# Optimization experiments

Hardware: AMD Instinct MI355X
Metric: run time of the kernel (lower is better)

Reference implementation:

```python
import jax, jax.numpy as jnp
import numpy as np

N_NODES = 100000
N_EDGES = 3200000
IN_FEAT = 512
HIDDEN = 16
N_CLASSES = 7


def gcn_conv(x, src, dst, dinv, W, b, n):
    # x: [N, Fin], src/dst: [E+N] (self-loops appended), dinv: [E+N already-indexed? no]
    h = x @ W  # [N, Fout]
    norm = (dinv[src] * dinv[dst])[:, None]  # [E+N, 1]
    msg = h[src] * norm
    out = jax.ops.segment_sum(msg, dst, num_segments=n)
    return out + b


def setup_inputs() -> dict:
    key = jax.random.key(0)
    k1, k2, k3, k4 = jax.random.split(key, 4)
    x = jax.random.normal(k1, (N_NODES, IN_FEAT), dtype=jnp.float32)
    edge_index = jax.random.randint(k2, (2, N_EDGES), 0, N_NODES, dtype=jnp.int64)
    # Glorot-style init for GCNConv linear layers
    W1 = jax.random.normal(k3, (IN_FEAT, HIDDEN), dtype=jnp.float32) / np.sqrt(IN_FEAT)
    b1 = jnp.zeros((HIDDEN,), dtype=jnp.float32)
    W2 = jax.random.normal(k4, (HIDDEN, N_CLASSES), dtype=jnp.float32) / np.sqrt(HIDDEN)
    b2 = jnp.zeros((N_CLASSES,), dtype=jnp.float32)
    return {"x": x, "edge_index": edge_index, "W1": W1, "b1": b1, "W2": W2, "b2": b2}


def reference(x, edge_index, W1, b1, W2, b2):
    n = x.shape[0]
    loop = jnp.arange(n, dtype=edge_index.dtype)
    src = jnp.concatenate([edge_index[0], loop])  # add self-loops (PyG default)
    dst = jnp.concatenate([edge_index[1], loop])
    # symmetric normalization: deg computed on destination with self-loops
    deg = jax.ops.segment_sum(jnp.ones_like(dst, dtype=x.dtype), dst, num_segments=n)
    dinv = jnp.where(deg > 0, jax.lax.rsqrt(deg), 0.0)
    h = gcn_conv(x, src, dst, dinv, W1, b1, n)
    h = jax.nn.relu(h)
    h = gcn_conv(h, src, dst, dinv, W2, b2, n)
    return jax.nn.log_softmax(h, axis=1)
```

## Files before the change

kernel.cpp:

```cpp
#include <hip/hip_runtime.h>

#define IN_FEAT 512
#define HID 16
#define NC 7

#define NPB    128
#define NPB_SH 7
#define NBMAX  1024
#define CAPB   5120
#define CAPS   8192
#define P1_EDGES 8192
#define P1_EPT   32

__global__ __launch_bounds__(256) void k_binmm(const int* __restrict__ src,
                                               const int* __restrict__ dst,
                                               int* __restrict__ gcur,
                                               int* __restrict__ binned,
                                               const float* __restrict__ x,
                                               const float* __restrict__ W,
                                               float* __restrict__ h1,
                                               int E, int NB, int nchunk, int n) {
    int tid = threadIdx.x;
    if ((int)blockIdx.x < nchunk) {
        __shared__ int lcur[NBMAX];
        __shared__ int sbase[NBMAX];
        for (int b = tid; b < NB; b += 256) lcur[b] = 0;
        __syncthreads();

        int base = blockIdx.x * P1_EDGES + tid;
        int d[P1_EPT];
        int lp[P1_EPT];
#pragma unroll
        for (int i = 0; i < P1_EPT; ++i) {
            int e = base + i * 256;
            d[i] = (e < E) ? __builtin_nontemporal_load(dst + e) : -1;
        }
#pragma unroll
        for (int i = 0; i < P1_EPT; ++i) {
            if (d[i] >= 0) lp[i] = atomicAdd(&lcur[d[i] >> NPB_SH], 1);
        }
        __syncthreads();
        for (int b = tid; b < NB; b += 256) {
            int c = lcur[b];
            sbase[b] = c ? atomicAdd(&gcur[b], c) : 0;
        }
        __syncthreads();
#pragma unroll
        for (int i = 0; i < P1_EPT; ++i) {
            if (d[i] < 0) continue;
            int e = base + i * 256;
            int s = __builtin_nontemporal_load(src + e);
            int b = d[i] >> NPB_SH;
            int pos = sbase[b] + lp[i];
            if (pos < CAPB)
                binned[(size_t)b * CAPB + pos] = s | ((d[i] & (NPB - 1)) << 20);
        }
    } else {
        int row = ((int)blockIdx.x - nchunk) * 256 + tid;
        if (row >= n) return;
        const float4* xr = reinterpret_cast<const float4*>(x + (size_t)row * IN_FEAT);
        float acc[HID];
#pragma unroll
        for (int c = 0; c < HID; ++c) acc[c] = 0.0f;
        for (int kt0 = 0; kt0 < IN_FEAT / 4; kt0 += 8) {
            float4 xv[8];
#pragma unroll
            for (int j = 0; j < 8; ++j) xv[j] = xr[kt0 + j];
#pragma unroll
            for (int j = 0; j < 8; ++j) {
                const float* wk = W + (size_t)(kt0 + j) * 4 * HID;
#pragma unroll
                for (int c = 0; c < HID; ++c) acc[c] = fmaf(xv[j].x, wk[c], acc[c]);
#pragma unroll
                for (int c = 0; c < HID; ++c) acc[c] = fmaf(xv[j].y, wk[HID + c], acc[c]);
#pragma unroll
                for (int c = 0; c < HID; ++c) acc[c] = fmaf(xv[j].z, wk[2 * HID + c], acc[c]);
#pragma unroll
                for (int c = 0; c < HID; ++c) acc[c] = fmaf(xv[j].w, wk[3 * HID + c], acc[c]);
            }
        }
        float4* hp = reinterpret_cast<float4*>(h1 + (size_t)row * HID);
#pragma unroll
        for (int j = 0; j < 4; ++j)
            hp[j] = make_float4(acc[4 * j], acc[4 * j + 1], acc[4 * j + 2], acc[4 * j + 3]);
    }
}

__global__ __launch_bounds__(256) void k_sort2(const int* __restrict__ binned,
                                               const int* __restrict__ gcur,
                                               int* __restrict__ off,
                                               float* __restrict__ dinv,
                                               int* __restrict__ csr,
                                               const int* __restrict__ src,
                                               const int* __restrict__ dst,
                                               int n, int E, int NB) {
    __shared__ int hist[NPB];
    __shared__ int hoff[NPB];
    __shared__ int cur[NPB];
    __shared__ int wtot[4];
    __shared__ int s_base;
    __shared__ int stage[CAPS];
    int b = blockIdx.x;
    int lo = b << NPB_SH;
    int nn = min(NPB, n - lo);
    int tid = threadIdx.x;
    int lane = tid & 63, wid = tid >> 6;
    int tot = gcur[b];

    int pre = 0;
    for (int k = tid; k < b; k += 256) pre += gcur[k];
#pragma unroll
    for (int o = 32; o >= 1; o >>= 1) pre += __shfl_xor(pre, o, 64);
    if (lane == 0) wtot[wid] = pre;
    if (tid < NPB) { hist[tid] = 0; cur[tid] = 0; }
    __syncthreads();
    if (tid == 0) s_base = wtot[0] + wtot[1] + wtot[2] + wtot[3];
    __syncthreads();
    int base = s_base;
    bool fits = (tot <= CAPB) && (tot <= CAPS);

    const int* bb = binned + (size_t)b * CAPB;
    if (fits) {
        for (int k = tid; k < tot; k += 256)
            atomicAdd(&hist[(bb[k] >> 20) & (NPB - 1)], 1);
    } else {
        for (int e = tid; e < E; e += 256) {
            int dd = dst[e];
            if ((dd >> NPB_SH) == b) atomicAdd(&hist[dd & (NPB - 1)], 1);
        }
    }
    __syncthreads();

    int v = 0, incl = 0;
    if (tid < NPB) {
        v = hist[tid];
        incl = v;
#pragma unroll
        for (int o = 1; o < 64; o <<= 1) {
            int t = __shfl_up(incl, o, 64);
            if ((tid & 63) >= o) incl += t;
        }
        if ((tid & 63) == 63) wtot[tid >> 6] = incl;
    }
    __syncthreads();
    if (tid < NPB) {
        int ex = incl - v + ((tid >= 64) ? wtot[0] : 0);
        hoff[tid] = ex;
        if (tid < nn) {
            off[lo + tid] = base + ex;
            dinv[lo + tid] = rsqrtf((float)v + 1.0f);
        }
    }
    if (b == NB - 1 && tid == 0) off[n] = base + tot;
    __syncthreads();

    if (fits) {
        for (int k = tid; k < tot; k += 256) {
            int e = bb[k];
            int dl = (e >> 20) & (NPB - 1);
            int p = hoff[dl] + atomicAdd(&cur[dl], 1);
            stage[p] = e & 0xFFFFF;
        }
        __syncthreads();
        for (int k = tid; k < tot; k += 256) csr[base + k] = stage[k];
    } else {
        for (int e = tid; e < E; e += 256) {
            int dd = dst[e];
            if ((dd >> NPB_SH) == b) {
                int dl = dd & (NPB - 1);
                int p = base + hoff[dl] + atomicAdd(&cur[dl], 1);
                csr[p] = src[e];
            }
        }
    }
}

__global__ void k_gather1(const float* __restrict__ h1, const int* __restrict__ csr_src,
                          const int* __restrict__ off, const float* __restrict__ dinv,
                          const float* __restrict__ b1, const float* __restrict__ W2,
                          float* __restrict__ h2, int n) {
    int t = blockIdx.x * blockDim.x + threadIdx.x;
    int v = t >> 2, part = t & 3;
    if (v >= n) return;
    float di = dinv[v];
    float4 hv = reinterpret_cast<const float4*>(h1 + (size_t)v * HID)[part];
    float dw = di * di;
    float4 acc = make_float4(hv.x * dw, hv.y * dw, hv.z * dw, hv.w * dw);
    int beg = off[v], end = off[v + 1];
    for (int i = beg; i < end; ++i) {
        int s = csr_src[i];
        float w = dinv[s] * di;
        float4 hs = reinterpret_cast<const float4*>(h1 + (size_t)s * HID)[part];
        acc.x = fmaf(hs.x, w, acc.x);
        acc.y = fmaf(hs.y, w, acc.y);
        acc.z = fmaf(hs.z, w, acc.z);
        acc.w = fmaf(hs.w, w, acc.w);
    }
    float tt[4];
    tt[0] = fmaxf(acc.x + b1[part * 4 + 0], 0.0f);
    tt[1] = fmaxf(acc.y + b1[part * 4 + 1], 0.0f);
    tt[2] = fmaxf(acc.z + b1[part * 4 + 2], 0.0f);
    tt[3] = fmaxf(acc.w + b1[part * 4 + 3], 0.0f);
    float o[NC];
#pragma unroll
    for (int c = 0; c < NC; ++c) o[c] = 0.0f;
#pragma unroll
    for (int j = 0; j < 4; ++j) {
        int k = part * 4 + j;
#pragma unroll
        for (int c = 0; c < NC; ++c) o[c] = fmaf(tt[j], W2[k * NC + c], o[c]);
    }
#pragma unroll
    for (int c = 0; c < NC; ++c) {
        o[c] += __shfl_xor(o[c], 1);
        o[c] += __shfl_xor(o[c], 2);
    }
    float4* hp = reinterpret_cast<float4*>(h2 + (size_t)v * 8);
    if (part == 0) hp[0] = make_float4(o[0], o[1], o[2], o[3]);
    if (part == 1) hp[1] = make_float4(o[4], o[5], o[6], 0.0f);
}

__global__ void k_gather2(const float* __restrict__ h2, const int* __restrict__ csr_src,
                          const int* __restrict__ off, const float* __restrict__ dinv,
                          const float* __restrict__ b2, float* __restrict__ out, int n) {
    int v = blockIdx.x * blockDim.x + threadIdx.x;
    if (v >= n) return;
    float di = dinv[v];
    float dw = di * di;
    const float4* hr = reinterpret_cast<const float4*>(h2 + (size_t)v * 8);
    float4 s0 = hr[0], s1 = hr[1];
    float4 a0 = make_float4(s0.x * dw, s0.y * dw, s0.z * dw, s0.w * dw);
    float4 a1 = make_float4(s1.x * dw, s1.y * dw, s1.z * dw, 0.0f);
    int beg = off[v], end = off[v + 1];
    for (int i = beg; i < end; ++i) {
        int s = csr_src[i];
        float w = dinv[s] * di;
        const float4* hs = reinterpret_cast<const float4*>(h2 + (size_t)s * 8);
        float4 v0 = hs[0], v1 = hs[1];
        a0.x = fmaf(v0.x, w, a0.x);
        a0.y = fmaf(v0.y, w, a0.y);
        a0.z = fmaf(v0.z, w, a0.z);
        a0.w = fmaf(v0.w, w, a0.w);
        a1.x = fmaf(v1.x, w, a1.x);
        a1.y = fmaf(v1.y, w, a1.y);
        a1.z = fmaf(v1.z, w, a1.z);
    }
    float z[NC];
    z[0] = a0.x + b2[0]; z[1] = a0.y + b2[1]; z[2] = a0.z + b2[2]; z[3] = a0.w + b2[3];
    z[4] = a1.x + b2[4]; z[5] = a1.y + b2[5]; z[6] = a1.z + b2[6];
    float m = z[0];
#pragma unroll
    for (int c = 1; c < NC; ++c) m = fmaxf(m, z[c]);
    float sum = 0.0f;
#pragma unroll
    for (int c = 0; c < NC; ++c) sum += expf(z[c] - m);
    float lse = logf(sum) + m;
#pragma unroll
    for (int c = 0; c < NC; ++c) out[(size_t)v * NC + c] = z[c] - lse;
}

extern "C" void kernel_launch(void* const* d_in, const int* in_sizes, int n_in,
                              void* d_out, int out_size, void* d_ws, size_t ws_size,
                              hipStream_t stream) {
    const float* x  = (const float*)d_in[0];
    const int*   ei = (const int*)d_in[1];
    const float* W1 = (const float*)d_in[2];
    const float* b1 = (const float*)d_in[3];
    const float* W2 = (const float*)d_in[4];
    const float* b2 = (const float*)d_in[5];

    int n = in_sizes[0] / IN_FEAT;
    int E = in_sizes[1] / 2;
    const int* src = ei;
    const int* dst = ei + E;
    int NB = (n + NPB - 1) >> NPB_SH;

    char* p = (char*)d_ws;
    int*   binned  = (int*)p;     p += (size_t)NB * CAPB * sizeof(int);
    float* h1      = (float*)p;   p += (size_t)HID * n * sizeof(float);
    float* h2      = (float*)p;   p += (size_t)8 * n * sizeof(float);
    int*   csr_src = (int*)p;     p += (size_t)E * sizeof(int);
    int*   gcur    = (int*)p;     p += (size_t)NBMAX * sizeof(int);
    int*   off     = (int*)p;     p += (size_t)(n + 1) * sizeof(int);
    float* dinv    = (float*)p;   p += (size_t)n * sizeof(float);

    const int tb = 256;
    int gN = (n + tb - 1) / tb;
    int gN4 = (4 * n + tb - 1) / tb;
    int nchunk = (E + P1_EDGES - 1) / P1_EDGES;

    hipMemsetAsync(gcur, 0, (size_t)NBMAX * sizeof(int), stream);
    k_binmm  <<<nchunk + gN, tb, 0, stream>>>(src, dst, gcur, binned, x, W1, h1,
                                              E, NB, nchunk, n);
    k_sort2  <<<NB, tb, 0, stream>>>(binned, gcur, off, dinv, csr_src,
                                     src, dst, n, E, NB);
    k_gather1<<<gN4, tb, 0, stream>>>(h1, csr_src, off, dinv, b1, W2, h2, n);
    k_gather2<<<gN,  tb, 0, stream>>>(h2, csr_src, off, dinv, b2, (float*)d_out, n);
}
```

Baseline: 253.5 us.

## Replace CSR sort with per-bin shared-memory atomic aggregation

Drops building a full CSR (prefix sums, offsets, staged scatter). Each destination bin is now aggregated straight from the binned edge list into shared-memory accumulators with LDS float atomics. The degree histogram becomes a small separate kernel, and both gather layers run one block per 128-node bin. This removes the CSR write and reread and the offset computation, at the cost of LDS atomic contention and a summation order that is no longer deterministic.

```diff
diff --git a/kernel.cpp b/kernel.cpp
--- a/kernel.cpp
+++ b/kernel.cpp
@@ -8,7 +8,6 @@
 #define NPB_SH 7
 #define NBMAX  1024
 #define CAPB   5120
-#define CAPS   8192
 #define P1_EDGES 8192
 #define P1_EPT   32
 
@@ -86,41 +85,20 @@
     }
 }
 
-__global__ __launch_bounds__(256) void k_sort2(const int* __restrict__ binned,
-                                               const int* __restrict__ gcur,
-                                               int* __restrict__ off,
-                                               float* __restrict__ dinv,
-                                               int* __restrict__ csr,
-                                               const int* __restrict__ src,
-                                               const int* __restrict__ dst,
-                                               int n, int E, int NB) {
+__global__ __launch_bounds__(256) void k_hist(const int* __restrict__ binned,
+                                              const int* __restrict__ gcur,
+                                              float* __restrict__ dinv,
+                                              const int* __restrict__ dst,
+                                              int n, int E) {
     __shared__ int hist[NPB];
-    __shared__ int hoff[NPB];
-    __shared__ int cur[NPB];
-    __shared__ int wtot[4];
-    __shared__ int s_base;
-    __shared__ int stage[CAPS];
-    int b = blockIdx.x;
+    int b = blockIdx.x, tid = threadIdx.x;
     int lo = b << NPB_SH;
     int nn = min(NPB, n - lo);
-    int tid = threadIdx.x;
-    int lane = tid & 63, wid = tid >> 6;
     int tot = gcur[b];
-
-    int pre = 0;
-    for (int k = tid; k < b; k += 256) pre += gcur[k];
-#pragma unroll
-    for (int o = 32; o >= 1; o >>= 1) pre += __shfl_xor(pre, o, 64);
-    if (lane == 0) wtot[wid] = pre;
-    if (tid < NPB) { hist[tid] = 0; cur[tid] = 0; }
-    __syncthreads();
-    if (tid == 0) s_base = wtot[0] + wtot[1] + wtot[2] + wtot[3];
-    __syncthreads();
-    int base = s_base;
-    bool fits = (tot <= CAPB) && (tot <= CAPS);
-
-    const int* bb = binned + (size_t)b * CAPB;
-    if (fits) {
+    if (tid < NPB) hist[tid] = 0;
+    __syncthreads();
+    if (tot <= CAPB) {
+        const int* bb = binned + (size_t)b * CAPB;
         for (int k = tid; k < tot; k += 256)
             atomicAdd(&hist[(bb[k] >> 20) & (NPB - 1)], 1);
     } else {
@@ -130,133 +108,165 @@
         }
     }
     __syncthreads();
-
-    int v = 0, incl = 0;
-    if (tid < NPB) {
-        v = hist[tid];
-        incl = v;
-#pragma unroll
-        for (int o = 1; o < 64; o <<= 1) {
-            int t = __shfl_up(incl, o, 64);
-            if ((tid & 63) >= o) incl += t;
-        }
-        if ((tid & 63) == 63) wtot[tid >> 6] = incl;
-    }
-    __syncthreads();
-    if (tid < NPB) {
-        int ex = incl - v + ((tid >= 64) ? wtot[0] : 0);
-        hoff[tid] = ex;
-        if (tid < nn) {
-            off[lo + tid] = base + ex;
-            dinv[lo + tid] = rsqrtf((float)v + 1.0f);
-        }
-    }
-    if (b == NB - 1 && tid == 0) off[n] = base + tot;
-    __syncthreads();
-
-    if (fits) {
-        for (int k = tid; k < tot; k += 256) {
+    if (tid < nn) dinv[lo + tid] = rsqrtf((float)hist[tid] + 1.0f);
+}
+
+__global__ __launch_bounds__(256) void k_gather1b(const int* __restrict__ binned,
+                                                  const int* __restrict__ gcur,
+                                                  const float* __restrict__ h1,
+                                                  const float* __restrict__ dinv,
+                                                  const float* __restrict__ b1,
+                                                  const float* __restrict__ W2,
+                                                  float* __restrict__ h2,
+                                                  const int* __restrict__ src,
+                                                  const int* __restrict__ dst,
+                                                  int n, int E) {
+    __shared__ float acc[NPB][HID];
+    int b = blockIdx.x, tid = threadIdx.x;
+    int lo = b << NPB_SH;
+    int nn = min(NPB, n - lo);
+    int tot = gcur[b];
+
+    for (int q = tid; q < nn * 4; q += 256) {
+        int v = q >> 2, part = q & 3;
+        float di = dinv[lo + v];
+        float dw = di * di;
+        float4 hv = reinterpret_cast<const float4*>(h1 + (size_t)(lo + v) * HID)[part];
+        acc[v][part * 4 + 0] = hv.x * dw;
+        acc[v][part * 4 + 1] = hv.y * dw;
+        acc[v][part * 4 + 2] = hv.z * dw;
+        acc[v][part * 4 + 3] = hv.w * dw;
+    }
+    __syncthreads();
+
+    int part = tid & 3;
+    if (tot <= CAPB) {
+        const int* bb = binned + (size_t)b * CAPB;
+        for (int k = tid >> 2; k < tot; k += 64) {
             int e = bb[k];
+            int s = e & 0xFFFFF;
             int dl = (e >> 20) & (NPB - 1);
-            int p = hoff[dl] + atomicAdd(&cur[dl], 1);
-            stage[p] = e & 0xFFFFF;
-        }
-        __syncthreads();
-        for (int k = tid; k < tot; k += 256) csr[base + k] = stage[k];
+            float w = dinv[s] * dinv[lo + dl];
+            float4 hs = reinterpret_cast<const float4*>(h1 + (size_t)s * HID)[part];
+            atomicAdd(&acc[dl][part * 4 + 0], hs.x * w);
+            atomicAdd(&acc[dl][part * 4 + 1], hs.y * w);
+            atomicAdd(&acc[dl][part * 4 + 2], hs.z * w);
+            atomicAdd(&acc[dl][part * 4 + 3], hs.w * w);
+        }
     } else {
-        for (int e = tid; e < E; e += 256) {
-            int dd = dst[e];
-            if ((dd >> NPB_SH) == b) {
-                int dl = dd & (NPB - 1);
-                int p = base + hoff[dl] + atomicAdd(&cur[dl], 1);
-                csr[p] = src[e];
-            }
-        }
-    }
-}
-
-__global__ void k_gather1(const float* __restrict__ h1, const int* __restrict__ csr_src,
-                          const int* __restrict__ off, const float* __restrict__ dinv,
-                          const float* __restrict__ b1, const float* __restrict__ W2,
-                          float* __restrict__ h2, int n) {
-    int t = blockIdx.x * blockDim.x + threadIdx.x;
-    int v = t >> 2, part = t & 3;
-    if (v >= n) return;
-    float di = dinv[v];
-    float4 hv = reinterpret_cast<const float4*>(h1 + (size_t)v * HID)[part];
-    float dw = di * di;
-    float4 acc = make_float4(hv.x * dw, hv.y * dw, hv.z * dw, hv.w * dw);
-    int beg = off[v], end = off[v + 1];
-    for (int i = beg; i < end; ++i) {
-        int s = csr_src[i];
-        float w = dinv[s] * di;
-        float4 hs = reinterpret_cast<const float4*>(h1 + (size_t)s * HID)[part];
-        acc.x = fmaf(hs.x, w, acc.x);
-        acc.y = fmaf(hs.y, w, acc.y);
-        acc.z = fmaf(hs.z, w, acc.z);
-        acc.w = fmaf(hs.w, w, acc.w);
-    }
-    float tt[4];
-    tt[0] = fmaxf(acc.x + b1[part * 4 + 0], 0.0f);
-    tt[1] = fmaxf(acc.y + b1[part * 4 + 1], 0.0f);
-    tt[2] = fmaxf(acc.z + b1[part * 4 + 2], 0.0f);
-    tt[3] = fmaxf(acc.w + b1[part * 4 + 3], 0.0f);
-    float o[NC];
-#pragma unroll
-    for (int c = 0; c < NC; ++c) o[c] = 0.0f;
-#pragma unroll
-    for (int j = 0; j < 4; ++j) {
-        int k = part * 4 + j;
-#pragma unroll
-        for (int c = 0; c < NC; ++c) o[c] = fmaf(tt[j], W2[k * NC + c], o[c]);
-    }
-#pragma unroll
-    for (int c = 0; c < NC; ++c) {
-        o[c] += __shfl_xor(o[c], 1);
-        o[c] += __shfl_xor(o[c], 2);
-    }
-    float4* hp = reinterpret_cast<float4*>(h2 + (size_t)v * 8);
-    if (part == 0) hp[0] = make_float4(o[0], o[1], o[2], o[3]);
-    if (part == 1) hp[1] = make_float4(o[4], o[5], o[6], 0.0f);
-}
-
-__global__ void k_gather2(const float* __restrict__ h2, const int* __restrict__ csr_src,
-                          const int* __restrict__ off, const float* __restrict__ dinv,
-                          const float* __restrict__ b2, float* __restrict__ out, int n) {
-    int v = blockIdx.x * blockDim.x + threadIdx.x;
-    if (v >= n) return;
-    float di = dinv[v];
-    float dw = di * di;
-    const float4* hr = reinterpret_cast<const float4*>(h2 + (size_t)v * 8);
-    float4 s0 = hr[0], s1 = hr[1];
-    float4 a0 = make_float4(s0.x * dw, s0.y * dw, s0.z * dw, s0.w * dw);
-    float4 a1 = make_float4(s1.x * dw, s1.y * dw, s1.z * dw, 0.0f);
-    int beg = off[v], end = off[v + 1];
-    for (int i = beg; i < end; ++i) {
-        int s = csr_src[i];
-        float w = dinv[s] * di;
-        const float4* hs = reinterpret_cast<const float4*>(h2 + (size_t)s * 8);
-        float4 v0 = hs[0], v1 = hs[1];
-        a0.x = fmaf(v0.x, w, a0.x);
-        a0.y = fmaf(v0.y, w, a0.y);
-        a0.z = fmaf(v0.z, w, a0.z);
-        a0.w = fmaf(v0.w, w, a0.w);
-        a1.x = fmaf(v1.x, w, a1.x);
-        a1.y = fmaf(v1.y, w, a1.y);
-        a1.z = fmaf(v1.z, w, a1.z);
-    }
-    float z[NC];
-    z[0] = a0.x + b2[0]; z[1] = a0.y + b2[1]; z[2] = a0.z + b2[2]; z[3] = a0.w + b2[3];
-    z[4] = a1.x + b2[4]; z[5] = a1.y + b2[5]; z[6] = a1.z + b2[6];
-    float m = z[0];
-#pragma unroll
-    for (int c = 1; c < NC; ++c) m = fmaxf(m, z[c]);
-    float sum = 0.0f;
-#pragma unroll
-    for (int c = 0; c < NC; ++c) sum += expf(z[c] - m);
-    float lse = logf(sum) + m;
-#pragma unroll
-    for (int c = 0; c < NC; ++c) out[(size_t)v * NC + c] = z[c] - lse;
+        for (int k = tid >> 2; k < E; k += 64) {
+            int dd = dst[k];
+            if ((dd >> NPB_SH) != b) continue;
+            int s = src[k];
+            int dl = dd & (NPB - 1);
+            float w = dinv[s] * dinv[lo + dl];
+            float4 hs = reinterpret_cast<const float4*>(h1 + (size_t)s * HID)[part];
+            atomicAdd(&acc[dl][part * 4 + 0], hs.x * w);
+            atomicAdd(&acc[dl][part * 4 + 1], hs.y * w);
+            atomicAdd(&acc[dl][part * 4 + 2], hs.z * w);
+            atomicAdd(&acc[dl][part * 4 + 3], hs.w * w);
+        }
+    }
+    __syncthreads();
+
+    for (int q = tid; q < nn * 4; q += 256) {
+        int v = q >> 2;
+        int pt = q & 3;
+        float tt[4];
+#pragma unroll
+        for (int j = 0; j < 4; ++j)
+            tt[j] = fmaxf(acc[v][pt * 4 + j] + b1[pt * 4 + j], 0.0f);
+        float o[NC];
+#pragma unroll
+        for (int c = 0; c < NC; ++c) o[c] = 0.0f;
+#pragma unroll
+        for (int j = 0; j < 4; ++j) {
+            int k = pt * 4 + j;
+#pragma unroll
+            for (int c = 0; c < NC; ++c) o[c] = fmaf(tt[j], W2[k * NC + c], o[c]);
+        }
+#pragma unroll
+        for (int c = 0; c < NC; ++c) {
+            o[c] += __shfl_xor(o[c], 1);
+            o[c] += __shfl_xor(o[c], 2);
+        }
+        float4* hp = reinterpret_cast<float4*>(h2 + (size_t)(lo + v) * 8);
+        if (pt == 0) hp[0] = make_float4(o[0], o[1], o[2], o[3]);
+        if (pt == 1) hp[1] = make_float4(o[4], o[5], o[6], 0.0f);
+    }
+}
+
+__global__ __launch_bounds__(256) void k_gather2b(const int* __restrict__ binned,
+                                                  const int* __restrict__ gcur,
+                                                  const float* __restrict__ h2,
+                                                  const float* __restrict__ dinv,
+                                                  const float* __restrict__ b2,
+                                                  float* __restrict__ out,
+                                                  const int* __restrict__ src,
+                                                  const int* __restrict__ dst,
+                                                  int n, int E) {
+    __shared__ float acc[NPB][8];
+    int b = blockIdx.x, tid = threadIdx.x;
+    int lo = b << NPB_SH;
+    int nn = min(NPB, n - lo);
+    int tot = gcur[b];
+
+    for (int q = tid; q < nn * 2; q += 256) {
+        int v = q >> 1, part = q & 1;
+        float di = dinv[lo + v];
+        float dw = di * di;
+        float4 hv = reinterpret_cast<const float4*>(h2 + (size_t)(lo + v) * 8)[part];
+        acc[v][part * 4 + 0] = hv.x * dw;
+        acc[v][part * 4 + 1] = hv.y * dw;
+        acc[v][part * 4 + 2] = hv.z * dw;
+        acc[v][part * 4 + 3] = hv.w * dw;
+    }
+    __syncthreads();
+
+    int part = tid & 1;
+    if (tot <= CAPB) {
+        const int* bb = binned + (size_t)b * CAPB;
+        for (int k = tid >> 1; k < tot; k += 128) {
+            int e = bb[k];
+            int s = e & 0xFFFFF;
+            int dl = (e >> 20) & (NPB - 1);
+            float w = dinv[s] * dinv[lo + dl];
+            float4 hs = reinterpret_cast<const float4*>(h2 + (size_t)s * 8)[part];
+            atomicAdd(&acc[dl][part * 4 + 0], hs.x * w);
+            atomicAdd(&acc[dl][part * 4 + 1], hs.y * w);
+            atomicAdd(&acc[dl][part * 4 + 2], hs.z * w);
+            if (part == 0) atomicAdd(&acc[dl][3], hs.w * w);
+        }
+    } else {
+        for (int k = tid >> 1; k < E; k += 128) {
+            int dd = dst[k];
+            if ((dd >> NPB_SH) != b) continue;
+            int s = src[k];
+            int dl = dd & (NPB - 1);
+            float w = dinv[s] * dinv[lo + dl];
+            float4 hs = reinterpret_cast<const float4*>(h2 + (size_t)s * 8)[part];
+            atomicAdd(&acc[dl][part * 4 + 0], hs.x * w);
+            atomicAdd(&acc[dl][part * 4 + 1], hs.y * w);
+            atomicAdd(&acc[dl][part * 4 + 2], hs.z * w);
+            if (part == 0) atomicAdd(&acc[dl][3], hs.w * w);
+        }
+    }
+    __syncthreads();
+
+    if (tid < nn) {
+        float z[NC];
+#pragma unroll
+        for (int c = 0; c < NC; ++c) z[c] = acc[tid][c] + b2[c];
+        float m = z[0];
+#pragma unroll
+        for (int c = 1; c < NC; ++c) m = fmaxf(m, z[c]);
+        float sum = 0.0f;
+#pragma unroll
+        for (int c = 0; c < NC; ++c) sum += expf(z[c] - m);
+        float lse = logf(sum) + m;
+#pragma unroll
+        for (int c = 0; c < NC; ++c) out[(size_t)(lo + tid) * NC + c] = z[c] - lse;
+    }
 }
 
 extern "C" void kernel_launch(void* const* d_in, const int* in_sizes, int n_in,
@@ -276,24 +286,20 @@
     int NB = (n + NPB - 1) >> NPB_SH;
 
     char* p = (char*)d_ws;
-    int*   binned  = (int*)p;     p += (size_t)NB * CAPB * sizeof(int);
-    float* h1      = (float*)p;   p += (size_t)HID * n * sizeof(float);
-    float* h2      = (float*)p;   p += (size_t)8 * n * sizeof(float);
-    int*   csr_src = (int*)p;     p += (size_t)E * sizeof(int);
-    int*   gcur    = (int*)p;     p += (size_t)NBMAX * sizeof(int);
-    int*   off     = (int*)p;     p += (size_t)(n + 1) * sizeof(int);
-    float* dinv    = (float*)p;   p += (size_t)n * sizeof(float);
+    int*   binned = (int*)p;    p += (size_t)NB * CAPB * sizeof(int);
+    float* h1     = (float*)p;  p += (size_t)HID * n * sizeof(float);
+    float* h2     = (float*)p;  p += (size_t)8 * n * sizeof(float);
+    int*   gcur   = (int*)p;    p += (size_t)NBMAX * sizeof(int);
+    float* dinv   = (float*)p;  p += (size_t)n * sizeof(float);
 
     const int tb = 256;
     int gN = (n + tb - 1) / tb;
-    int gN4 = (4 * n + tb - 1) / tb;
     int nchunk = (E + P1_EDGES - 1) / P1_EDGES;
 
     hipMemsetAsync(gcur, 0, (size_t)NBMAX * sizeof(int), stream);
-    k_binmm  <<<nchunk + gN, tb, 0, stream>>>(src, dst, gcur, binned, x, W1, h1,
-                                              E, NB, nchunk, n);
-    k_sort2  <<<NB, tb, 0, stream>>>(binned, gcur, off, dinv, csr_src,
-                                     src, dst, n, E, NB);
-    k_gather1<<<gN4, tb, 0, stream>>>(h1, csr_src, off, dinv, b1, W2, h2, n);
-    k_gather2<<<gN,  tb, 0, stream>>>(h2, csr_src, off, dinv, b2, (float*)d_out, n);
-}
+    k_binmm   <<<nchunk + gN, tb, 0, stream>>>(src, dst, gcur, binned, x, W1, h1,
+                                               E, NB, nchunk, n);
+    k_hist    <<<NB, tb, 0, stream>>>(binned, gcur, dinv, dst, n, E);
+    k_gather1b<<<NB, tb, 0, stream>>>(binned, gcur, h1, dinv, b1, W2, h2, src, dst, n, E);
+    k_gather2b<<<NB, tb, 0, stream>>>(binned, gcur, h2, dinv, b2, (float*)d_out, src, dst, n, E);
+}
```

Result: slower. 598.6 us (+136.1%).
